# Performance work log

Measured on AMD Instinct MI355X. Metric: run time of the kernel, lower is better.

The kernel has to match this reference:

```python
import jax, jax.numpy as jnp
import numpy as np

NUM_HEAD = 4
HIDDEN = 128
NEG = 9e15


def _mha(x, maskf, wq, bq, wk, bk, wv, bv, wo, bo):
    # DGN-style multi-head attention: relu on q/k/v projections, mask-multiplied
    # scores with -9e15 fill on masked entries, relu on output projection.
    bs, n, _ = x.shape
    dh = HIDDEN // NUM_HEAD
    def proj(w, b):
        return jax.nn.relu(x @ w.T + b).reshape(bs, n, NUM_HEAD, dh).transpose(0, 2, 1, 3)
    q, k, v = proj(wq, bq), proj(wk, bk), proj(wv, bv)  # [bs,H,n,dh]
    scores = jnp.einsum('bhnd,bhmd->bhnm', q, k) / jnp.sqrt(jnp.asarray(dh, x.dtype))
    m = maskf[:, None]  # [bs,1,n,n]
    scores = scores * m - NEG * (1.0 - m)
    att = jax.nn.softmax(scores, axis=-1)
    out = jnp.einsum('bhnm,bhmd->bhnd', att, v).transpose(0, 2, 1, 3).reshape(bs, n, HIDDEN)
    return jax.nn.relu(out @ wo.T + bo), att


def _gru_cell(xin, h, w_ih, w_hh, b_ih, b_hh):
    gi = xin @ w_ih.T + b_ih  # [N, 3*hidden]
    gh = h @ w_hh.T + b_hh
    i_r, i_z, i_n = jnp.split(gi, 3, axis=-1)
    h_r, h_z, h_n = jnp.split(gh, 3, axis=-1)
    r = jax.nn.sigmoid(i_r + h_r)
    z = jax.nn.sigmoid(i_z + h_z)
    n = jnp.tanh(i_n + r * h_n)
    return (1.0 - z) * n + z * h


def setup_inputs() -> dict:
    key = jax.random.key(0)
    ks = jax.random.split(key, 20)
    bs, n_ant, in_dim, hd, act = 4096, 64, 64, 128, 20
    s = 0.05
    x = jax.random.normal(ks[0], (bs, n_ant, in_dim), jnp.float32)
    mask = jax.random.randint(ks[1], (bs, n_ant, n_ant), 0, 2, jnp.int32)
    eye = jnp.eye(n_ant, dtype=jnp.int32)[None]
    mask = jnp.maximum(mask, eye)  # ensure self-edges so no softmax row is fully masked
    hidden_state = jax.random.normal(ks[2], (bs, n_ant, hd), jnp.float32)
    def w(k, shape):
        return jax.random.normal(k, shape, jnp.float32) * s
    return dict(
        x=x, mask=mask, hidden_state=hidden_state,
        enc_w=w(ks[3], (hd, in_dim)), enc_b=jnp.zeros((hd,), jnp.float32),
        q1_w=w(ks[4], (hd, hd)), q1_b=jnp.zeros((hd,), jnp.float32),
        k1_w=w(ks[5], (hd, hd)), k1_b=jnp.zeros((hd,), jnp.float32),
        v1_w=w(ks[6], (hd, hd)), v1_b=jnp.zeros((hd,), jnp.float32),
        o1_w=w(ks[7], (hd, hd)), o1_b=jnp.zeros((hd,), jnp.float32),
        q2_w=w(ks[8], (hd, hd)), q2_b=jnp.zeros((hd,), jnp.float32),
        k2_w=w(ks[9], (hd, hd)), k2_b=jnp.zeros((hd,), jnp.float32),
        v2_w=w(ks[10], (hd, hd)), v2_b=jnp.zeros((hd,), jnp.float32),
        o2_w=w(ks[11], (hd, hd)), o2_b=jnp.zeros((hd,), jnp.float32),
        gru_w_ih=w(ks[12], (3 * hd, hd)), gru_w_hh=w(ks[13], (3 * hd, hd)),
        gru_b_ih=jnp.zeros((3 * hd,), jnp.float32), gru_b_hh=jnp.zeros((3 * hd,), jnp.float32),
        lin_w=w(ks[14], (act, hd)), lin_b=jnp.zeros((act,), jnp.float32),
    )


def reference(x, mask, hidden_state,
              enc_w, enc_b,
              q1_w, q1_b, k1_w, k1_b, v1_w, v1_b, o1_w, o1_b,
              q2_w, q2_b, k2_w, k2_b, v2_w, v2_b, o2_w, o2_b,
              gru_w_ih, gru_w_hh, gru_b_ih, gru_b_hh,
              lin_w, lin_b):
    bs, n_ant, _ = x.shape
    maskf = mask.astype(x.dtype)
    xe = jax.nn.relu(x @ enc_w.T + enc_b)                     # [bs,n,hidden]
    h1, _ = _mha(xe, maskf, q1_w, q1_b, k1_w, k1_b, v1_w, v1_b, o1_w, o1_b)
    h2, _ = _mha(h1, maskf, q2_w, q2_b, k2_w, k2_b, v2_w, v2_b, o2_w, o2_b)
    h2f = h2.reshape(bs * n_ant, HIDDEN)
    hf = hidden_state.reshape(bs * n_ant, HIDDEN)
    h3 = _gru_cell(h2f, hf, gru_w_ih, gru_w_hh, gru_b_ih, gru_b_hh).reshape(bs, n_ant, HIDDEN)
    qs = h3 @ lin_w.T + lin_b                                 # with_non_linearity=False
    return qs, h3
```

## Files before the change

### kernel.cpp

```cpp
#include <hip/hip_runtime.h>
#include <hip/hip_bf16.h>

typedef unsigned int u32;
typedef unsigned short u16;
typedef unsigned long long u64;

using bf16x8 = __attribute__((ext_vector_type(8))) short;
using f32x4  = __attribute__((ext_vector_type(4))) float;
typedef float f4v __attribute__((ext_vector_type(4)));

#define NUNITS 31
#define WS_BIAS_OFF (NUNITS*8192)
#define NBIAS 1952

__device__ __forceinline__ u32 pk2(float a, float b){
    __hip_bfloat162 h = __float22bfloat162_rn(make_float2(a, b));
    union { __hip_bfloat162 h2; u32 u; } cv; cv.h2 = h; return cv.u;
}
__device__ __forceinline__ float b2f(u16 v){ return __uint_as_float(((u32)v) << 16); }
__device__ __forceinline__ int swch(int chunk, int key){ return (chunk & ~7) | ((chunk ^ key) & 7); }

__global__ __launch_bounds__(256) void convert_weights(
    const float* __restrict__ enc_w,
    const float* __restrict__ q1, const float* __restrict__ k1,
    const float* __restrict__ v1, const float* __restrict__ o1,
    const float* __restrict__ q2, const float* __restrict__ k2,
    const float* __restrict__ v2, const float* __restrict__ o2,
    const float* __restrict__ gih, const float* __restrict__ ghh,
    const float* __restrict__ lin,
    const float* __restrict__ enc_b,
    const float* __restrict__ q1b, const float* __restrict__ k1b,
    const float* __restrict__ v1b, const float* __restrict__ o1b,
    const float* __restrict__ q2b, const float* __restrict__ k2b,
    const float* __restrict__ v2b, const float* __restrict__ o2b,
    const float* __restrict__ gbih, const float* __restrict__ gbhh,
    const float* __restrict__ linb,
    u16* __restrict__ dst)
{
    int idx = blockIdx.x*256 + threadIdx.x;
    if (idx < NUNITS*8192){
        int u = idx >> 13, rem = idx & 8191;
        int row = rem >> 6, ci = rem & 63;
        int p = ci >> 3, e = ci & 7;
        int lc = (((p ^ (row & 7)) & 7) << 3) | e;
        float val;
        if (u == 0){
            val = enc_w[row*64 + lc];
        } else if (u <= 16){
            int v = u - 1; int L = v >> 3; int r8 = v & 7;
            int mat, kh;
            if (r8 < 6){ mat = r8 % 3; kh = r8 / 3; } else { mat = 3; kh = r8 - 6; }
            const float* s;
            if (L == 0){ s = (mat==0)?q1:(mat==1)?k1:(mat==2)?v1:o1; }
            else       { s = (mat==0)?q2:(mat==1)?k2:(mat==2)?v2:o2; }
            val = s[row*128 + kh*64 + lc];
        } else if (u <= 28){
            int v = u - 17;
            int gate, kh; const float* s;
            if (v < 8){ gate = v & 1; kh = (v >> 1) & 1; s = (v >= 4) ? ghh : gih; }
            else      { int w8 = v - 8; gate = 2; kh = w8 & 1; s = (w8 >= 2) ? ghh : gih; }
            val = s[(gate*128 + row)*128 + kh*64 + lc];
        } else {
            int kh = u - 29;
            val = (row < 20) ? lin[row*128 + kh*64 + lc] : 0.f;
        }
        __hip_bfloat16 hv = __float2bfloat16(val);
        union { __hip_bfloat16 h; u16 us; } cv; cv.h = hv;
        dst[idx] = cv.us;
    } else if (idx < NUNITS*8192 + NBIAS){
        int i = idx - NUNITS*8192;
        float val;
        if      (i < 128)  val = enc_b[i];
        else if (i < 256)  val = q1b[i-128];
        else if (i < 384)  val = k1b[i-256];
        else if (i < 512)  val = v1b[i-384];
        else if (i < 640)  val = o1b[i-512];
        else if (i < 768)  val = q2b[i-640];
        else if (i < 896)  val = k2b[i-768];
        else if (i < 1024) val = v2b[i-896];
        else if (i < 1152) val = o2b[i-1024];
        else if (i < 1536) val = gbih[i-1152];
        else if (i < 1920) val = gbhh[i-1536];
        else if (i < 1940) val = linb[i-1920];
        else               val = 0.f;
        ((float*)(dst + NUNITS*8192))[i] = val;
    }
}

#define BARX() do{ asm volatile("s_waitcnt lgkmcnt(0)" ::: "memory"); \
                   __builtin_amdgcn_s_barrier(); \
                   asm volatile("" ::: "memory"); }while(0)
#define WAITV(N) asm volatile("s_waitcnt vmcnt(" #N ")" ::: "memory")

template<int U>
__device__ __forceinline__ void issue_unit(const u16* Wu, u16* WBs, int tid){
    u16* slot = WBs + (U & 1) * 8192;
    const u16* src = Wu + U * 8192;
    #pragma unroll
    for (int t = 0; t < 4; t++){
        __builtin_amdgcn_global_load_lds(
            (const __attribute__((address_space(1))) void*)(src + t*2048 + tid*8),
            (__attribute__((address_space(3))) void*)(slot + t*2048 + tid*8),
            16, 0, 0);
    }
}
#define SLOTC(U) (WBs + ((U) & 1) * 8192)

template<int U, bool ISSUE>
__device__ __forceinline__ void phase_pre(const u16* Wu, u16* WBs, int tid){
    BARX();
    if constexpr (ISSUE){
        issue_unit<U+1>(Wu, WBs, tid);
        WAITV(4);
    } else {
        WAITV(0);
    }
    BARX();
}

template<int M,int N>
__device__ __forceinline__ void zacc(f32x4 (&a)[M][N]){
    #pragma unroll
    for (int i=0;i<M;i++)
        #pragma unroll
        for (int j=0;j<N;j++) a[i][j] = (f32x4){0.f,0.f,0.f,0.f};
}

struct XF { bf16x8 f[4][2]; };

__device__ __forceinline__ void loadX(XF& xf, const u16* X, int kh, int c, int g){
    const int key = c & 7;
    #pragma unroll
    for (int kk = 0; kk < 2; kk++){
        const int pw = (kk*4 + g) ^ key;
        #pragma unroll
        for (int j = 0; j < 4; j++)
            xf.f[j][kk] = *(const bf16x8*)(X + (j*16 + c)*128 + (kh*8 + pw)*8);
    }
}

__device__ __forceinline__ void wgemmR(const u16* Wb, const XF& xf,
                                       int w, int c, int g, f32x4 (&acc)[2][4]){
    const int key = c & 7;
    __builtin_amdgcn_s_setprio(1);
    #pragma unroll
    for (int kk = 0; kk < 2; kk++){
        const int pw = (kk*4 + g) ^ key;
        bf16x8 a0 = *(const bf16x8*)(Wb + ((w*2+0)*16 + c)*64 + pw*8);
        bf16x8 a1 = *(const bf16x8*)(Wb + ((w*2+1)*16 + c)*64 + pw*8);
        #pragma unroll
        for (int j = 0; j < 4; j++){
            acc[0][j] = __builtin_amdgcn_mfma_f32_16x16x32_bf16(a0, xf.f[j][kk], acc[0][j], 0,0,0);
            acc[1][j] = __builtin_amdgcn_mfma_f32_16x16x32_bf16(a1, xf.f[j][kk], acc[1][j], 0,0,0);
        }
    }
    __builtin_amdgcn_s_setprio(0);
}

__device__ __forceinline__ void vgemmR(const u16* Wb, const XF& xf,
                                       int w, int c, int g, f32x4 (&acc)[4][2]){
    const int key = c & 7;
    __builtin_amdgcn_s_setprio(1);
    #pragma unroll
    for (int kk = 0; kk < 2; kk++){
        const int pw = (kk*4 + g) ^ key;
        bf16x8 b0 = *(const bf16x8*)(Wb + ((w*2+0)*16 + c)*64 + pw*8);
        bf16x8 b1 = *(const bf16x8*)(Wb + ((w*2+1)*16 + c)*64 + pw*8);
        #pragma unroll
        for (int i = 0; i < 4; i++){
            acc[i][0] = __builtin_amdgcn_mfma_f32_16x16x32_bf16(xf.f[i][kk], b0, acc[i][0], 0,0,0);
            acc[i][1] = __builtin_amdgcn_mfma_f32_16x16x32_bf16(xf.f[i][kk], b1, acc[i][1], 0,0,0);
        }
    }
    __builtin_amdgcn_s_setprio(0);
}

__device__ __forceinline__ void epiW(f32x4 (&acc)[2][4], float4 bv0, float4 bv1,
                                     u16* dst, int w, int c, int g){
    const int key = c & 7;
    #pragma unroll
    for (int i = 0; i < 2; i++){
        float4 bv = i ? bv1 : bv0;
        const int col0 = (w*2+i)*16 + g*4;
        const int coff = swch(col0>>3, key)*8 + (col0&7);
        #pragma unroll
        for (int j = 0; j < 4; j++){
            int row = j*16 + c;
            float v0 = fmaxf(acc[i][j][0]+bv.x, 0.f);
            float v1 = fmaxf(acc[i][j][1]+bv.y, 0.f);
            float v2 = fmaxf(acc[i][j][2]+bv.z, 0.f);
            float v3 = fmaxf(acc[i][j][3]+bv.w, 0.f);
            uint2 o; o.x = pk2(v0,v1); o.y = pk2(v2,v3);
            *(uint2*)(dst + row*128 + coff) = o;
        }
    }
}

template<int LAYER>
__device__ __forceinline__ void mha_layer(const u16* Wu, u16* WBs,
                                          u16* ACT, u16* QXp, u16* KPp,
                                          const float* wsb, const float* h0, size_t rowbase,
                                          int tid, int w, int c, int g, const u64* mbits)
{
    constexpr int UB = 1 + LAYER*8;
    constexpr int BB = 128 + LAYER*512;
    const int key = c & 7;
    const int col00 = w*32 + g*4;
    const int col01 = col00 + 16;

    XF xf;
    f32x4 accQ[2][4], accK[2][4];
    f32x4 vacc[4][2];

    phase_pre<UB+0, true>(Wu, WBs, tid);
    zacc(accQ); zacc(accK); zacc(vacc);
    loadX(xf, ACT, 0, c, g);
    wgemmR(SLOTC(UB+0), xf, w, c, g, accQ);

    phase_pre<UB+1, true>(Wu, WBs, tid);
    wgemmR(SLOTC(UB+1), xf, w, c, g, accK);

    phase_pre<UB+2, true>(Wu, WBs, tid);
    vgemmR(SLOTC(UB+2), xf, w, c, g, vacc);

    float4 bq0 = *(const float4*)(wsb + BB + col00);
    float4 bq1 = *(const float4*)(wsb + BB + col01);
    phase_pre<UB+3, true>(Wu, WBs, tid);
    loadX(xf, ACT, 1, c, g);
    wgemmR(SLOTC(UB+3), xf, w, c, g, accQ);
    epiW(accQ, bq0, bq1, QXp, w, c, g);

    float4 bk0 = *(const float4*)(wsb + BB + 128 + col00);
    float4 bk1 = *(const float4*)(wsb + BB + 128 + col01);
    phase_pre<UB+4, true>(Wu, WBs, tid);
    wgemmR(SLOTC(UB+4), xf, w, c, g, accK);
    epiW(accK, bk0, bk1, KPp, w, c, g);

    float bv0 = wsb[BB + 256 + w*32 + c];
    float bv1 = wsb[BB + 256 + w*32 + 16 + c];
    phase_pre<UB+5, true>(Wu, WBs, tid);
    vgemmR(SLOTC(UB+5), xf, w, c, g, vacc);

    #pragma unroll
    for (int j = 0; j < 2; j++){
        int vrow = w*32 + j*16 + c;
        float bv = j ? bv1 : bv0;
        #pragma unroll
        for (int i = 0; i < 4; i++){
            int kk = i >> 1, p = i & 1;
            float v0 = fmaxf(vacc[i][j][0]+bv, 0.f);
            float v1 = fmaxf(vacc[i][j][1]+bv, 0.f);
            float v2 = fmaxf(vacc[i][j][2]+bv, 0.f);
            float v3 = fmaxf(vacc[i][j][3]+bv, 0.f);
            uint2 o; o.x = pk2(v0,v1); o.y = pk2(v2,v3);
            *(uint2*)(ACT + vrow*64 + swch(kk*4+g, key)*8 + p*4) = o;
        }
    }

    const int h = w;
    f32x4 sc[4][4];
    {
        bf16x8 kf[4];
        #pragma unroll
        for (int kt = 0; kt < 4; kt++)
            kf[kt] = *(const bf16x8*)(KPp + (kt*16 + c)*128 + swch(h*4+g, key)*8);
        __builtin_amdgcn_s_setprio(1);
        #pragma unroll
        for (int qt = 0; qt < 4; qt++){
            bf16x8 qf = *(const bf16x8*)(QXp + (qt*16 + c)*128 + swch(h*4+g, key)*8);
            #pragma unroll
            for (int kt = 0; kt < 4; kt++){
                f32x4 z4 = (f32x4){0.f,0.f,0.f,0.f};
                sc[qt][kt] = __builtin_amdgcn_mfma_f32_16x16x32_bf16(kf[kt], qf, z4, 0,0,0);
            }
        }
        __builtin_amdgcn_s_setprio(0);
    }
    BARX();

    f4v hr[8];
    if (LAYER == 1){
        const float* hp = h0 + (rowbase + (tid>>2))*128 + (tid&3)*32;
        #pragma unroll
        for (int t = 0; t < 8; t++)
            hr[t] = __builtin_nontemporal_load((const f4v*)(hp + t*4));
    }

    {
        u32 pp[4][4][2];
        #pragma unroll
        for (int qt = 0; qt < 4; qt++){
            u64 mb = mbits[qt];
            float mx = -1e30f;
            #pragma unroll
            for (int kt = 0; kt < 4; kt++)
                #pragma unroll
                for (int r = 0; r < 4; r++){
                    float s = sc[qt][kt][r] * 0.17677669529663687f;
                    s = ((mb >> (kt*16 + g*4 + r)) & 1ull) ? s : -1e30f;
                    sc[qt][kt][r] = s;
                    mx = fmaxf(mx, s);
                }
            mx = fmaxf(mx, __shfl_xor(mx, 16));
            mx = fmaxf(mx, __shfl_xor(mx, 32));
            float sum = 0.f;
            #pragma unroll
            for (int kt = 0; kt < 4; kt++)
                #pragma unroll
                for (int r = 0; r < 4; r++){
                    float e = __expf(sc[qt][kt][r] - mx);
                    sc[qt][kt][r] = e; sum += e;
                }
            sum += __shfl_xor(sum, 16);
            sum += __shfl_xor(sum, 32);
            float inv = 1.f / sum;
            #pragma unroll
            for (int kt = 0; kt < 4; kt++){
                pp[qt][kt][0] = pk2(sc[qt][kt][0]*inv, sc[qt][kt][1]*inv);
                pp[qt][kt][1] = pk2(sc[qt][kt][2]*inv, sc[qt][kt][3]*inv);
            }
        }
        #pragma unroll
        for (int dt = 0; dt < 2; dt++){
            f32x4 pa[4];
            #pragma unroll
            for (int qt = 0; qt < 4; qt++) pa[qt] = (f32x4){0.f,0.f,0.f,0.f};
            #pragma unroll
            for (int kk = 0; kk < 2; kk++){
                bf16x8 vt = *(const bf16x8*)(ACT + (h*32 + dt*16 + c)*64 + ((kk*4+g)^key)*8);
                __builtin_amdgcn_s_setprio(1);
                #pragma unroll
                for (int qt = 0; qt < 4; qt++){
                    union { u32 u4[4]; bf16x8 v8; } bbv;
                    bbv.u4[0]=pp[qt][kk*2][0];   bbv.u4[1]=pp[qt][kk*2][1];
                    bbv.u4[2]=pp[qt][kk*2+1][0]; bbv.u4[3]=pp[qt][kk*2+1][1];
                    pa[qt] = __builtin_amdgcn_mfma_f32_16x16x32_bf16(vt, bbv.v8, pa[qt], 0,0,0);
                }
                __builtin_amdgcn_s_setprio(0);
            }
            #pragma unroll
            for (int qt = 0; qt < 4; qt++){
                int col = h*32 + dt*16 + g*4;
                uint2 o; o.x = pk2(pa[qt][0], pa[qt][1]); o.y = pk2(pa[qt][2], pa[qt][3]);
                *(uint2*)(QXp + (qt*16 + c)*128 + swch(col>>3, key)*8 + (col&7)) = o;
            }
        }
    }

    if (LAYER == 1){
        int hrow = tid >> 2, seg = tid & 3;
        #pragma unroll
        for (int cc = 0; cc < 4; cc++){
            int p = seg*4 + cc;
            int ps = (p & 8) | ((p ^ (hrow & 7)) & 7);
            f4v fa = hr[cc*2], fb = hr[cc*2+1];
            uint4 o; o.x = pk2(fa.x,fa.y); o.y = pk2(fa.z,fa.w);
            o.z = pk2(fb.x,fb.y); o.w = pk2(fb.z,fb.w);
            *(uint4*)(KPp + hrow*128 + ps*8) = o;
        }
    }

    f32x4 acc[2][4];
    phase_pre<UB+6, true>(Wu, WBs, tid);
    zacc(acc);
    loadX(xf, QXp, 0, c, g);
    wgemmR(SLOTC(UB+6), xf, w, c, g, acc);

    float4 bo0 = *(const float4*)(wsb + BB + 384 + col00);
    float4 bo1 = *(const float4*)(wsb + BB + 384 + col01);
    phase_pre<UB+7, true>(Wu, WBs, tid);
    loadX(xf, QXp, 1, c, g);
    wgemmR(SLOTC(UB+7), xf, w, c, g, acc);
    epiW(acc, bo0, bo1, ACT, w, c, g);
}

__global__ __launch_bounds__(256, 2) void drgn_pipe(
    const float* __restrict__ x, const int* __restrict__ maskg,
    const float* __restrict__ h0, const u16* __restrict__ W16,
    float* __restrict__ out_qs, float* __restrict__ out_h3)
{
    __shared__ __align__(16) u16 SMEM[40960];
    u16* ACT = SMEM;
    u16* QXp = SMEM + 8192;
    u16* KPp = SMEM + 16384;
    u16* WBs = SMEM + 24576;

    const int tid = threadIdx.x;
    const int w = tid >> 6, lane = tid & 63;
    const int c = lane & 15, g = lane >> 4;
    const int key = c & 7;
    const size_t rowbase = (size_t)blockIdx.x * 64;
    const u16* Wu = W16;
    const float* wsb = (const float*)(W16 + WS_BIAS_OFF);
    const int col00 = w*32 + g*4;
    const int col01 = col00 + 16;

    u64* MrowT = (u64*)KPp;
    #pragma unroll 4
    for (int rr = 0; rr < 16; rr++){
        int row = w*16 + rr;
        int mv = __builtin_nontemporal_load(maskg + (rowbase + row)*64 + lane);
        u64 bits = __ballot(mv != 0);
        if (lane == 0) MrowT[row] = bits;
    }
    for (int i = tid; i < 512; i += 256){
        int row = i >> 3, p = i & 7;
        int lc = (p ^ (row & 7)) & 7;
        const float* sp = x + (rowbase + row)*64 + lc*8;
        f4v f0 = __builtin_nontemporal_load((const f4v*)sp);
        f4v f1 = __builtin_nontemporal_load((const f4v*)(sp + 4));
        uint4 o; o.x = pk2(f0.x,f0.y); o.y = pk2(f0.z,f0.w);
        o.z = pk2(f1.x,f1.y); o.w = pk2(f1.z,f1.w);
        *(uint4*)(QXp + row*128 + p*8) = o;
    }
    __syncthreads();
    u64 mbits[4];
    #pragma unroll
    for (int qt = 0; qt < 4; qt++) mbits[qt] = MrowT[qt*16 + c];

    issue_unit<0>(Wu, WBs, tid);

    {
        XF xf;
        f32x4 acc[2][4];
        float4 b0 = *(const float4*)(wsb + col00);
        float4 b1 = *(const float4*)(wsb + col01);
        phase_pre<0, true>(Wu, WBs, tid);
        zacc(acc);
        loadX(xf, QXp, 0, c, g);
        wgemmR(SLOTC(0), xf, w, c, g, acc);
        epiW(acc, b0, b1, ACT, w, c, g);
    }

    mha_layer<0>(Wu, WBs, ACT, QXp, KPp, wsb, h0, rowbase, tid, w, c, g, mbits);
    mha_layer<1>(Wu, WBs, ACT, QXp, KPp, wsb, h0, rowbase, tid, w, c, g, mbits);

    XF xf;
    float rrA[2][4][4], zzA[2][4][4];
    {
        f32x4 aIr[2][4], aIz[2][4], aHr[2][4], aHz[2][4];
        phase_pre<17, true>(Wu, WBs, tid);
        zacc(aIr); zacc(aIz);
        loadX(xf, ACT, 0, c, g);
        wgemmR(SLOTC(17), xf, w, c, g, aIr);
        phase_pre<18, true>(Wu, WBs, tid);
        wgemmR(SLOTC(18), xf, w, c, g, aIz);
        phase_pre<19, true>(Wu, WBs, tid);
        loadX(xf, ACT, 1, c, g);
        wgemmR(SLOTC(19), xf, w, c, g, aIr);
        phase_pre<20, true>(Wu, WBs, tid);
        wgemmR(SLOTC(20), xf, w, c, g, aIz);

        phase_pre<21, true>(Wu, WBs, tid);
        zacc(aHr); zacc(aHz);
        loadX(xf, KPp, 0, c, g);
        wgemmR(SLOTC(21), xf, w, c, g, aHr);
        phase_pre<22, true>(Wu, WBs, tid);
        wgemmR(SLOTC(22), xf, w, c, g, aHz);
        float4 bir0 = *(const float4*)(wsb + 1152 + col00);
        float4 bir1 = *(const float4*)(wsb + 1152 + col01);
        float4 bhr0 = *(const float4*)(wsb + 1536 + col00);
        float4 bhr1 = *(const float4*)(wsb + 1536 + col01);
        phase_pre<23, true>(Wu, WBs, tid);
        loadX(xf, KPp, 1, c, g);
        wgemmR(SLOTC(23), xf, w, c, g, aHr);
        float4 biz0 = *(const float4*)(wsb + 1152 + 128 + col00);
        float4 biz1 = *(const float4*)(wsb + 1152 + 128 + col01);
        float4 bhz0 = *(const float4*)(wsb + 1536 + 128 + col00);
        float4 bhz1 = *(const float4*)(wsb + 1536 + 128 + col01);
        phase_pre<24, true>(Wu, WBs, tid);
        wgemmR(SLOTC(24), xf, w, c, g, aHz);

        #pragma unroll
        for (int i = 0; i < 2; i++){
            float4 bir = i ? bir1 : bir0; float4 bhr = i ? bhr1 : bhr0;
            float4 biz = i ? biz1 : biz0; float4 bhz = i ? bhz1 : bhz0;
            #pragma unroll
            for (int j = 0; j < 4; j++)
                #pragma unroll
                for (int r = 0; r < 4; r++){
                    rrA[i][j][r] = 1.f/(1.f + __expf(-(aIr[i][j][r] + (&bir.x)[r] + aHr[i][j][r] + (&bhr.x)[r])));
                    zzA[i][j][r] = 1.f/(1.f + __expf(-(aIz[i][j][r] + (&biz.x)[r] + aHz[i][j][r] + (&bhz.x)[r])));
                }
        }
    }
    {
        f32x4 aIn[2][4], aHn[2][4];
        phase_pre<25, true>(Wu, WBs, tid);
        zacc(aIn);
        loadX(xf, ACT, 0, c, g);
        wgemmR(SLOTC(25), xf, w, c, g, aIn);
        phase_pre<26, true>(Wu, WBs, tid);
        loadX(xf, ACT, 1, c, g);
        wgemmR(SLOTC(26), xf, w, c, g, aIn);
        phase_pre<27, true>(Wu, WBs, tid);
        zacc(aHn);
        loadX(xf, KPp, 0, c, g);
        wgemmR(SLOTC(27), xf, w, c, g, aHn);
        float4 bin0 = *(const float4*)(wsb + 1152 + 256 + col00);
        float4 bin1 = *(const float4*)(wsb + 1152 + 256 + col01);
        float4 bhn0 = *(const float4*)(wsb + 1536 + 256 + col00);
        float4 bhn1 = *(const float4*)(wsb + 1536 + 256 + col01);
        phase_pre<28, true>(Wu, WBs, tid);
        loadX(xf, KPp, 1, c, g);
        wgemmR(SLOTC(28), xf, w, c, g, aHn);

        #pragma unroll
        for (int i = 0; i < 2; i++){
            float4 bi = i ? bin1 : bin0; float4 bh = i ? bhn1 : bhn0;
            int col0 = w*32 + i*16 + g*4;
            int coff = swch(col0>>3, key)*8 + (col0&7);
            #pragma unroll
            for (int j = 0; j < 4; j++){
                int row = j*16 + c;
                uint2 hv = *(const uint2*)(KPp + row*128 + coff);
                float h0v[4] = { b2f((u16)(hv.x & 0xffffu)), b2f((u16)(hv.x >> 16)),
                                 b2f((u16)(hv.y & 0xffffu)), b2f((u16)(hv.y >> 16)) };
                f4v h3o;
                #pragma unroll
                for (int r = 0; r < 4; r++){
                    float xn = aIn[i][j][r] + (&bi.x)[r] + rrA[i][j][r]*(aHn[i][j][r] + (&bh.x)[r]);
                    float e2 = __expf(-2.f*fabsf(xn));
                    float th = (1.f - e2)/(1.f + e2);
                    th = (xn >= 0.f) ? th : -th;
                    float zv = zzA[i][j][r];
                    h3o[r] = (1.f - zv)*th + zv*h0v[r];
                }
                uint2 o; o.x = pk2(h3o[0],h3o[1]); o.y = pk2(h3o[2],h3o[3]);
                *(uint2*)(ACT + row*128 + coff) = o;
                __builtin_nontemporal_store(h3o, (f4v*)(out_h3 + (rowbase + row)*128 + col0));
            }
        }
    }

    {
        f32x4 qa[2][4];
        float4 lb0 = (col00 < 20) ? *(const float4*)(wsb + 1920 + col00) : (float4){0.f,0.f,0.f,0.f};
        float4 lb1 = (col01 < 20) ? *(const float4*)(wsb + 1920 + col01) : (float4){0.f,0.f,0.f,0.f};
        phase_pre<29, true>(Wu, WBs, tid);
        zacc(qa);
        loadX(xf, ACT, 0, c, g);
        wgemmR(SLOTC(29), xf, w, c, g, qa);
        phase_pre<30, false>(Wu, WBs, tid);
        loadX(xf, ACT, 1, c, g);
        wgemmR(SLOTC(30), xf, w, c, g, qa);

        #pragma unroll
        for (int i = 0; i < 2; i++){
            int col0 = w*32 + i*16 + g*4;
            if (col0 < 20){
                float4 lb = i ? lb1 : lb0;
                #pragma unroll
                for (int j = 0; j < 4; j++){
                    int row = j*16 + c;
                    f4v o;
                    o.x = qa[i][j][0]+lb.x; o.y = qa[i][j][1]+lb.y;
                    o.z = qa[i][j][2]+lb.z; o.w = qa[i][j][3]+lb.w;
                    __builtin_nontemporal_store(o, (f4v*)(out_qs + (rowbase + row)*20 + col0));
                }
            }
        }
    }
}

extern "C" void kernel_launch(void* const* d_in, const int* in_sizes, int n_in,
                              void* d_out, int out_size, void* d_ws, size_t ws_size,
                              hipStream_t stream) {
    const float* x     = (const float*)d_in[0];
    const int*   mask  = (const int*)  d_in[1];
    const float* h0    = (const float*)d_in[2];
    const float* enc_w = (const float*)d_in[3];
    const float* enc_b = (const float*)d_in[4];
    const float* q1_w  = (const float*)d_in[5];  const float* q1_b = (const float*)d_in[6];
    const float* k1_w  = (const float*)d_in[7];  const float* k1_b = (const float*)d_in[8];
    const float* v1_w  = (const float*)d_in[9];  const float* v1_b = (const float*)d_in[10];
    const float* o1_w  = (const float*)d_in[11]; const float* o1_b = (const float*)d_in[12];
    const float* q2_w  = (const float*)d_in[13]; const float* q2_b = (const float*)d_in[14];
    const float* k2_w  = (const float*)d_in[15]; const float* k2_b = (const float*)d_in[16];
    const float* v2_w  = (const float*)d_in[17]; const float* v2_b = (const float*)d_in[18];
    const float* o2_w  = (const float*)d_in[19]; const float* o2_b = (const float*)d_in[20];
    const float* gwih  = (const float*)d_in[21]; const float* gwhh = (const float*)d_in[22];
    const float* gbih  = (const float*)d_in[23]; const float* gbhh = (const float*)d_in[24];
    const float* lin_w = (const float*)d_in[25]; const float* lin_b = (const float*)d_in[26];

    const int bs = in_sizes[0] / (64 * 64);
    float* out_qs = (float*)d_out;
    float* out_h3 = out_qs + (size_t)bs * 64 * 20;
    u16* W16 = (u16*)d_ws;

    const int total = NUNITS*8192 + NBIAS;
    hipLaunchKernelGGL(convert_weights, dim3((total + 255) / 256), dim3(256), 0, stream,
                       enc_w, q1_w, k1_w, v1_w, o1_w, q2_w, k2_w, v2_w, o2_w,
                       gwih, gwhh, lin_w,
                       enc_b, q1_b, k1_b, v1_b, o1_b, q2_b, k2_b, v2_b, o2_b,
                       gbih, gbhh, lin_b, W16);
    hipLaunchKernelGGL(drgn_pipe, dim3(bs), dim3(256), 0, stream,
                       x, mask, h0, W16, out_qs, out_h3);
}
```

Before: 365.7 us.

## Load MFMA weight fragments directly into registers instead of staging through LDS

Weights are repacked at conversion time into per-wave, per-lane MFMA fragment order so each wave can fetch its operands straight from global or L2 into VGPRs. The LDS double-buffer and the two barriers per weight unit go away, leaving only the barriers the activation data needs, and loads are software-prefetched one or two units ahead. This frees 32 KB of LDS and removes many synchronisation points, at the cost of more VGPR pressure from holding several prefetched weight fragments. That pressure could cause spills or lower occupancy under the 2-block launch bound.

```diff
diff --git a/kernel.cpp b/kernel.cpp
--- a/kernel.cpp
+++ b/kernel.cpp
@@ -40,12 +40,16 @@
     int idx = blockIdx.x*256 + threadIdx.x;
     if (idx < NUNITS*8192){
         int u = idx >> 13, rem = idx & 8191;
-        int row = rem >> 6, ci = rem & 63;
-        int p = ci >> 3, e = ci & 7;
-        int lc = (((p ^ (row & 7)) & 7) << 3) | e;
+        int w = rem >> 11;
+        int t = (rem >> 9) & 3;
+        int l = (rem >> 3) & 63;
+        int e = idx & 7;
+        int i = t >> 1, kk = t & 1;
+        int oc = (w*2 + i)*16 + (l & 15);
+        int kl = kk*32 + (l >> 4)*8 + e;
         float val;
         if (u == 0){
-            val = enc_w[row*64 + lc];
+            val = enc_w[oc*64 + kl];
         } else if (u <= 16){
             int v = u - 1; int L = v >> 3; int r8 = v & 7;
             int mat, kh;
@@ -53,16 +57,16 @@
             const float* s;
             if (L == 0){ s = (mat==0)?q1:(mat==1)?k1:(mat==2)?v1:o1; }
             else       { s = (mat==0)?q2:(mat==1)?k2:(mat==2)?v2:o2; }
-            val = s[row*128 + kh*64 + lc];
+            val = s[oc*128 + kh*64 + kl];
         } else if (u <= 28){
             int v = u - 17;
             int gate, kh; const float* s;
             if (v < 8){ gate = v & 1; kh = (v >> 1) & 1; s = (v >= 4) ? ghh : gih; }
             else      { int w8 = v - 8; gate = 2; kh = w8 & 1; s = (w8 >= 2) ? ghh : gih; }
-            val = s[(gate*128 + row)*128 + kh*64 + lc];
+            val = s[(gate*128 + oc)*128 + kh*64 + kl];
         } else {
             int kh = u - 29;
-            val = (row < 20) ? lin[row*128 + kh*64 + lc] : 0.f;
+            val = (oc < 20) ? lin[oc*128 + kh*64 + kl] : 0.f;
         }
         __hip_bfloat16 hv = __float2bfloat16(val);
         union { __hip_bfloat16 h; u16 us; } cv; cv.h = hv;
@@ -90,32 +94,18 @@
 #define BARX() do{ asm volatile("s_waitcnt lgkmcnt(0)" ::: "memory"); \
                    __builtin_amdgcn_s_barrier(); \
                    asm volatile("" ::: "memory"); }while(0)
-#define WAITV(N) asm volatile("s_waitcnt vmcnt(" #N ")" ::: "memory")
+
+struct WB { bf16x8 a[4]; };
 
 template<int U>
-__device__ __forceinline__ void issue_unit(const u16* Wu, u16* WBs, int tid){
-    u16* slot = WBs + (U & 1) * 8192;
-    const u16* src = Wu + U * 8192;
-    #pragma unroll
-    for (int t = 0; t < 4; t++){
-        __builtin_amdgcn_global_load_lds(
-            (const __attribute__((address_space(1))) void*)(src + t*2048 + tid*8),
-            (__attribute__((address_space(3))) void*)(slot + t*2048 + tid*8),
-            16, 0, 0);
-    }
-}
-#define SLOTC(U) (WBs + ((U) & 1) * 8192)
-
-template<int U, bool ISSUE>
-__device__ __forceinline__ void phase_pre(const u16* Wu, u16* WBs, int tid){
-    BARX();
-    if constexpr (ISSUE){
-        issue_unit<U+1>(Wu, WBs, tid);
-        WAITV(4);
-    } else {
-        WAITV(0);
-    }
-    BARX();
+__device__ __forceinline__ WB load_unit(const u16* Wu, int w, int lane){
+    const u16* p = Wu + U*8192 + w*2048 + lane*8;
+    WB b;
+    b.a[0] = *(const bf16x8*)(p);
+    b.a[1] = *(const bf16x8*)(p + 512);
+    b.a[2] = *(const bf16x8*)(p + 1024);
+    b.a[3] = *(const bf16x8*)(p + 1536);
+    return b;
 }
 
 template<int M,int N>
@@ -139,37 +129,27 @@
     }
 }
 
-__device__ __forceinline__ void wgemmR(const u16* Wb, const XF& xf,
-                                       int w, int c, int g, f32x4 (&acc)[2][4]){
-    const int key = c & 7;
+__device__ __forceinline__ void wgemmW(const WB& wb, const XF& xf, f32x4 (&acc)[2][4]){
     __builtin_amdgcn_s_setprio(1);
     #pragma unroll
     for (int kk = 0; kk < 2; kk++){
-        const int pw = (kk*4 + g) ^ key;
-        bf16x8 a0 = *(const bf16x8*)(Wb + ((w*2+0)*16 + c)*64 + pw*8);
-        bf16x8 a1 = *(const bf16x8*)(Wb + ((w*2+1)*16 + c)*64 + pw*8);
         #pragma unroll
         for (int j = 0; j < 4; j++){
-            acc[0][j] = __builtin_amdgcn_mfma_f32_16x16x32_bf16(a0, xf.f[j][kk], acc[0][j], 0,0,0);
-            acc[1][j] = __builtin_amdgcn_mfma_f32_16x16x32_bf16(a1, xf.f[j][kk], acc[1][j], 0,0,0);
+            acc[0][j] = __builtin_amdgcn_mfma_f32_16x16x32_bf16(wb.a[kk],   xf.f[j][kk], acc[0][j], 0,0,0);
+            acc[1][j] = __builtin_amdgcn_mfma_f32_16x16x32_bf16(wb.a[2+kk], xf.f[j][kk], acc[1][j], 0,0,0);
         }
     }
     __builtin_amdgcn_s_setprio(0);
 }
 
-__device__ __forceinline__ void vgemmR(const u16* Wb, const XF& xf,
-                                       int w, int c, int g, f32x4 (&acc)[4][2]){
-    const int key = c & 7;
+__device__ __forceinline__ void vgemmW(const WB& wb, const XF& xf, f32x4 (&acc)[4][2]){
     __builtin_amdgcn_s_setprio(1);
     #pragma unroll
     for (int kk = 0; kk < 2; kk++){
-        const int pw = (kk*4 + g) ^ key;
-        bf16x8 b0 = *(const bf16x8*)(Wb + ((w*2+0)*16 + c)*64 + pw*8);
-        bf16x8 b1 = *(const bf16x8*)(Wb + ((w*2+1)*16 + c)*64 + pw*8);
         #pragma unroll
         for (int i = 0; i < 4; i++){
-            acc[i][0] = __builtin_amdgcn_mfma_f32_16x16x32_bf16(xf.f[i][kk], b0, acc[i][0], 0,0,0);
-            acc[i][1] = __builtin_amdgcn_mfma_f32_16x16x32_bf16(xf.f[i][kk], b1, acc[i][1], 0,0,0);
+            acc[i][0] = __builtin_amdgcn_mfma_f32_16x16x32_bf16(xf.f[i][kk], wb.a[kk],   acc[i][0], 0,0,0);
+            acc[i][1] = __builtin_amdgcn_mfma_f32_16x16x32_bf16(xf.f[i][kk], wb.a[2+kk], acc[i][1], 0,0,0);
         }
     }
     __builtin_amdgcn_s_setprio(0);
@@ -197,10 +177,10 @@
 }
 
 template<int LAYER>
-__device__ __forceinline__ void mha_layer(const u16* Wu, u16* WBs,
+__device__ __forceinline__ void mha_layer(const u16* Wu,
                                           u16* ACT, u16* QXp, u16* KPp,
                                           const float* wsb, const float* h0, size_t rowbase,
-                                          int tid, int w, int c, int g, const u64* mbits)
+                                          int tid, int w, int lane, int c, int g, const u64* mbits)
 {
     constexpr int UB = 1 + LAYER*8;
     constexpr int BB = 128 + LAYER*512;
@@ -212,34 +192,37 @@
     f32x4 accQ[2][4], accK[2][4];
     f32x4 vacc[4][2];
 
-    phase_pre<UB+0, true>(Wu, WBs, tid);
+    WB b_q0 = load_unit<UB+0>(Wu, w, lane);
+    WB b_k0 = load_unit<UB+1>(Wu, w, lane);
+    WB b_v0 = load_unit<UB+2>(Wu, w, lane);
+
     zacc(accQ); zacc(accK); zacc(vacc);
     loadX(xf, ACT, 0, c, g);
-    wgemmR(SLOTC(UB+0), xf, w, c, g, accQ);
-
-    phase_pre<UB+1, true>(Wu, WBs, tid);
-    wgemmR(SLOTC(UB+1), xf, w, c, g, accK);
-
-    phase_pre<UB+2, true>(Wu, WBs, tid);
-    vgemmR(SLOTC(UB+2), xf, w, c, g, vacc);
-
+    wgemmW(b_q0, xf, accQ);
+    WB b_q1 = load_unit<UB+3>(Wu, w, lane);
+    wgemmW(b_k0, xf, accK);
+    WB b_k1 = load_unit<UB+4>(Wu, w, lane);
+    vgemmW(b_v0, xf, vacc);
+    WB b_v1 = load_unit<UB+5>(Wu, w, lane);
+
+    loadX(xf, ACT, 1, c, g);
     float4 bq0 = *(const float4*)(wsb + BB + col00);
     float4 bq1 = *(const float4*)(wsb + BB + col01);
-    phase_pre<UB+3, true>(Wu, WBs, tid);
-    loadX(xf, ACT, 1, c, g);
-    wgemmR(SLOTC(UB+3), xf, w, c, g, accQ);
+    wgemmW(b_q1, xf, accQ);
+    WB b_o0 = load_unit<UB+6>(Wu, w, lane);
     epiW(accQ, bq0, bq1, QXp, w, c, g);
 
     float4 bk0 = *(const float4*)(wsb + BB + 128 + col00);
     float4 bk1 = *(const float4*)(wsb + BB + 128 + col01);
-    phase_pre<UB+4, true>(Wu, WBs, tid);
-    wgemmR(SLOTC(UB+4), xf, w, c, g, accK);
+    wgemmW(b_k1, xf, accK);
+    WB b_o1 = load_unit<UB+7>(Wu, w, lane);
     epiW(accK, bk0, bk1, KPp, w, c, g);
 
     float bv0 = wsb[BB + 256 + w*32 + c];
     float bv1 = wsb[BB + 256 + w*32 + 16 + c];
-    phase_pre<UB+5, true>(Wu, WBs, tid);
-    vgemmR(SLOTC(UB+5), xf, w, c, g, vacc);
+    vgemmW(b_v1, xf, vacc);
+
+    BARX();
 
     #pragma unroll
     for (int j = 0; j < 2; j++){
@@ -276,7 +259,6 @@
         }
         __builtin_amdgcn_s_setprio(0);
     }
-    BARX();
 
     f4v hr[8];
     if (LAYER == 1){
@@ -347,6 +329,8 @@
         }
     }
 
+    BARX();
+
     if (LAYER == 1){
         int hrow = tid >> 2, seg = tid & 3;
         #pragma unroll
@@ -361,17 +345,19 @@
     }
 
     f32x4 acc[2][4];
-    phase_pre<UB+6, true>(Wu, WBs, tid);
     zacc(acc);
     loadX(xf, QXp, 0, c, g);
-    wgemmR(SLOTC(UB+6), xf, w, c, g, acc);
-
+    wgemmW(b_o0, xf, acc);
+    WB b_n0 = load_unit<UB+8>(Wu, w, lane);
+    loadX(xf, QXp, 1, c, g);
     float4 bo0 = *(const float4*)(wsb + BB + 384 + col00);
     float4 bo1 = *(const float4*)(wsb + BB + 384 + col01);
-    phase_pre<UB+7, true>(Wu, WBs, tid);
-    loadX(xf, QXp, 1, c, g);
-    wgemmR(SLOTC(UB+7), xf, w, c, g, acc);
+    wgemmW(b_o1, xf, acc);
+    WB b_n1 = load_unit<UB+9>(Wu, w, lane);
     epiW(acc, bo0, bo1, ACT, w, c, g);
+    asm volatile("" :: "v"(b_n0.a[0]), "v"(b_n1.a[0]));
+
+    BARX();
 }
 
 __global__ __launch_bounds__(256, 2) void drgn_pipe(
@@ -379,11 +365,10 @@
     const float* __restrict__ h0, const u16* __restrict__ W16,
     float* __restrict__ out_qs, float* __restrict__ out_h3)
 {
-    __shared__ __align__(16) u16 SMEM[40960];
+    __shared__ __align__(16) u16 SMEM[24576];
     u16* ACT = SMEM;
     u16* QXp = SMEM + 8192;
     u16* KPp = SMEM + 16384;
-    u16* WBs = SMEM + 24576;
 
     const int tid = threadIdx.x;
     const int w = tid >> 6, lane = tid & 63;
@@ -413,64 +398,62 @@
         o.z = pk2(f1.x,f1.y); o.w = pk2(f1.z,f1.w);
         *(uint4*)(QXp + row*128 + p*8) = o;
     }
+    WB b_enc = load_unit<0>(Wu, w, lane);
     __syncthreads();
     u64 mbits[4];
     #pragma unroll
     for (int qt = 0; qt < 4; qt++) mbits[qt] = MrowT[qt*16 + c];
-
-    issue_unit<0>(Wu, WBs, tid);
 
     {
         XF xf;
         f32x4 acc[2][4];
         float4 b0 = *(const float4*)(wsb + col00);
         float4 b1 = *(const float4*)(wsb + col01);
-        phase_pre<0, true>(Wu, WBs, tid);
         zacc(acc);
         loadX(xf, QXp, 0, c, g);
-        wgemmR(SLOTC(0), xf, w, c, g, acc);
+        wgemmW(b_enc, xf, acc);
         epiW(acc, b0, b1, ACT, w, c, g);
     }
-
-    mha_layer<0>(Wu, WBs, ACT, QXp, KPp, wsb, h0, rowbase, tid, w, c, g, mbits);
-    mha_layer<1>(Wu, WBs, ACT, QXp, KPp, wsb, h0, rowbase, tid, w, c, g, mbits);
+    BARX();
+
+    mha_layer<0>(Wu, ACT, QXp, KPp, wsb, h0, rowbase, tid, w, lane, c, g, mbits);
+    mha_layer<1>(Wu, ACT, QXp, KPp, wsb, h0, rowbase, tid, w, lane, c, g, mbits);
 
     XF xf;
     float rrA[2][4][4], zzA[2][4][4];
     {
         f32x4 aIr[2][4], aIz[2][4], aHr[2][4], aHz[2][4];
-        phase_pre<17, true>(Wu, WBs, tid);
+        WB g17 = load_unit<17>(Wu, w, lane);
+        WB g18 = load_unit<18>(Wu, w, lane);
         zacc(aIr); zacc(aIz);
         loadX(xf, ACT, 0, c, g);
-        wgemmR(SLOTC(17), xf, w, c, g, aIr);
-        phase_pre<18, true>(Wu, WBs, tid);
-        wgemmR(SLOTC(18), xf, w, c, g, aIz);
-        phase_pre<19, true>(Wu, WBs, tid);
+        wgemmW(g17, xf, aIr);
+        WB g19 = load_unit<19>(Wu, w, lane);
+        wgemmW(g18, xf, aIz);
+        WB g20 = load_unit<20>(Wu, w, lane);
         loadX(xf, ACT, 1, c, g);
-        wgemmR(SLOTC(19), xf, w, c, g, aIr);
-        phase_pre<20, true>(Wu, WBs, tid);
-        wgemmR(SLOTC(20), xf, w, c, g, aIz);
-
-        phase_pre<21, true>(Wu, WBs, tid);
+        wgemmW(g19, xf, aIr);
+        WB g21 = load_unit<21>(Wu, w, lane);
+        wgemmW(g20, xf, aIz);
+        WB g22 = load_unit<22>(Wu, w, lane);
         zacc(aHr); zacc(aHz);
         loadX(xf, KPp, 0, c, g);
-        wgemmR(SLOTC(21), xf, w, c, g, aHr);
-        phase_pre<22, true>(Wu, WBs, tid);
-        wgemmR(SLOTC(22), xf, w, c, g, aHz);
+        wgemmW(g21, xf, aHr);
+        WB g23 = load_unit<23>(Wu, w, lane);
+        wgemmW(g22, xf, aHz);
+        WB g24 = load_unit<24>(Wu, w, lane);
+        loadX(xf, KPp, 1, c, g);
+        wgemmW(g23, xf, aHr);
+        wgemmW(g24, xf, aHz);
+
         float4 bir0 = *(const float4*)(wsb + 1152 + col00);
         float4 bir1 = *(const float4*)(wsb + 1152 + col01);
         float4 bhr0 = *(const float4*)(wsb + 1536 + col00);
         float4 bhr1 = *(const float4*)(wsb + 1536 + col01);
-        phase_pre<23, true>(Wu, WBs, tid);
-        loadX(xf, KPp, 1, c, g);
-        wgemmR(SLOTC(23), xf, w, c, g, aHr);
         float4 biz0 = *(const float4*)(wsb + 1152 + 128 + col00);
         float4 biz1 = *(const float4*)(wsb + 1152 + 128 + col01);
         float4 bhz0 = *(const float4*)(wsb + 1536 + 128 + col00);
         float4 bhz1 = *(const float4*)(wsb + 1536 + 128 + col01);
-        phase_pre<24, true>(Wu, WBs, tid);
-        wgemmR(SLOTC(24), xf, w, c, g, aHz);
-
         #pragma unroll
         for (int i = 0; i < 2; i++){
             float4 bir = i ? bir1 : bir0; float4 bhr = i ? bhr1 : bhr0;
@@ -484,26 +467,32 @@
                 }
         }
     }
+    WB g29, g30;
     {
         f32x4 aIn[2][4], aHn[2][4];
-        phase_pre<25, true>(Wu, WBs, tid);
+        WB g25 = load_unit<25>(Wu, w, lane);
+        WB g26 = load_unit<26>(Wu, w, lane);
         zacc(aIn);
         loadX(xf, ACT, 0, c, g);
-        wgemmR(SLOTC(25), xf, w, c, g, aIn);
-        phase_pre<26, true>(Wu, WBs, tid);
+        wgemmW(g25, xf, aIn);
+        WB g27 = load_unit<27>(Wu, w, lane);
         loadX(xf, ACT, 1, c, g);
-        wgemmR(SLOTC(26), xf, w, c, g, aIn);
-        phase_pre<27, true>(Wu, WBs, tid);
+        wgemmW(g26, xf, aIn);
+        WB g28 = load_unit<28>(Wu, w, lane);
         zacc(aHn);
         loadX(xf, KPp, 0, c, g);
-        wgemmR(SLOTC(27), xf, w, c, g, aHn);
+        wgemmW(g27, xf, aHn);
+        g29 = load_unit<29>(Wu, w, lane);
+        loadX(xf, KPp, 1, c, g);
+        wgemmW(g28, xf, aHn);
+        g30 = load_unit<30>(Wu, w, lane);
+
         float4 bin0 = *(const float4*)(wsb + 1152 + 256 + col00);
         float4 bin1 = *(const float4*)(wsb + 1152 + 256 + col01);
         float4 bhn0 = *(const float4*)(wsb + 1536 + 256 + col00);
         float4 bhn1 = *(const float4*)(wsb + 1536 + 256 + col01);
-        phase_pre<28, true>(Wu, WBs, tid);
-        loadX(xf, KPp, 1, c, g);
-        wgemmR(SLOTC(28), xf, w, c, g, aHn);
+
+        BARX();
 
         #pragma unroll
         for (int i = 0; i < 2; i++){
@@ -532,18 +521,17 @@
             }
         }
     }
+    BARX();
 
     {
         f32x4 qa[2][4];
         float4 lb0 = (col00 < 20) ? *(const float4*)(wsb + 1920 + col00) : (float4){0.f,0.f,0.f,0.f};
         float4 lb1 = (col01 < 20) ? *(const float4*)(wsb + 1920 + col01) : (float4){0.f,0.f,0.f,0.f};
-        phase_pre<29, true>(Wu, WBs, tid);
         zacc(qa);
         loadX(xf, ACT, 0, c, g);
-        wgemmR(SLOTC(29), xf, w, c, g, qa);
-        phase_pre<30, false>(Wu, WBs, tid);
+        wgemmW(g29, xf, qa);
         loadX(xf, ACT, 1, c, g);
-        wgemmR(SLOTC(30), xf, w, c, g, qa);
+        wgemmW(g30, xf, qa);
 
         #pragma unroll
         for (int i = 0; i < 2; i++){
```

Result: faster. 328.8 us (-10.1%).
